# Performance work log

Hardware: AMD Instinct MI355X
Metric: run time of the kernel (lower is better)

Reference implementation:

```python
import jax, jax.numpy as jnp
import numpy as np

H = 100  # hidden size of both LSTM layers (fixed in the module)

def lstm_layer(x, w_ih, w_hh, b_ih, b_hh):
    # x: [B, T, I]; w_ih: [4H, I]; w_hh: [4H, H]; biases: [4H]
    # PyTorch gate order: input, forget, cell(g), output.
    B, T, _ = x.shape
    xg = jnp.einsum('bti,gi->btg', x, w_ih) + b_ih + b_hh  # [B, T, 4H], input GEMM hoisted out of the scan
    h0 = jnp.zeros((B, H), x.dtype)
    c0 = jnp.zeros((B, H), x.dtype)
    w_hh_t = w_hh.T  # [H, 4H]

    def step(carry, xg_t):
        h, c = carry
        g = xg_t + h @ w_hh_t                # [B, 4H]
        i, f, gg, o = jnp.split(g, 4, axis=-1)
        i = jax.nn.sigmoid(i)
        f = jax.nn.sigmoid(f)
        gg = jnp.tanh(gg)
        o = jax.nn.sigmoid(o)
        c = f * c + i * gg
        h = o * jnp.tanh(c)
        return (h, c), h

    _, hs = jax.lax.scan(step, (h0, c0), jnp.swapaxes(xg, 0, 1))  # hs: [T, B, H]
    return jnp.swapaxes(hs, 0, 1)  # [B, T, H]


def setup_inputs() -> dict:
    key = jax.random.key(0)
    ks = jax.random.split(key, 13)
    B, T, I = 256, 2048, 8
    s = lambda fan: 1.0 / np.sqrt(fan)
    u = lambda k, shape, fan: jax.random.uniform(k, shape, jnp.float32, -s(fan), s(fan))
    return {
        'x': jax.random.normal(ks[0], (B, T, I), jnp.float32),
        'w_ih1': u(ks[1], (4 * H, I), H), 'w_hh1': u(ks[2], (4 * H, H), H),
        'b_ih1': u(ks[3], (4 * H,), H), 'b_hh1': u(ks[4], (4 * H,), H),
        'w_ih2': u(ks[5], (4 * H, H), H), 'w_hh2': u(ks[6], (4 * H, H), H),
        'b_ih2': u(ks[7], (4 * H,), H), 'b_hh2': u(ks[8], (4 * H,), H),
        'fc1_w': u(ks[9], (25, H), H), 'fc1_b': u(ks[10], (25,), H),
        'fc2_w': u(ks[11], (1, 25), 25), 'fc2_b': u(ks[12], (1,), 25),
    }


def reference(x, w_ih1, w_hh1, b_ih1, b_hh1, w_ih2, w_hh2, b_ih2, b_hh2,
              fc1_w, fc1_b, fc2_w, fc2_b):
    # Dropout layers are identity in eval mode.
    h1 = lstm_layer(x, w_ih1, w_hh1, b_ih1, b_hh1)    # [B, T, H]
    h2 = lstm_layer(h1, w_ih2, w_hh2, b_ih2, b_hh2)   # [B, T, H]
    last = h2[:, -1, :]                               # [B, H]
    y = last @ fc1_w.T + fc1_b                        # [B, 25]
    return y @ fc2_w.T + fc2_b                        # [B, 1]
```

## Files before the change

### kernel.cpp

```cpp
#include <hip/hip_runtime.h>

#define BB 256
#define TT 2048
#define HD 100
#define NGP 448

typedef _Float16 h2v __attribute__((ext_vector_type(2)));

__device__ __forceinline__ float fdot2s(unsigned w, unsigned h, float c) {
#if __has_builtin(__builtin_amdgcn_fdot2)
    return __builtin_amdgcn_fdot2(__builtin_bit_cast(h2v, w),
                                  __builtin_bit_cast(h2v, h), c, false);
#else
    h2v av = __builtin_bit_cast(h2v, w), bv = __builtin_bit_cast(h2v, h);
    c = fmaf((float)av[0], (float)bv[0], c);
    c = fmaf((float)av[1], (float)bv[1], c);
    return c;
#endif
}
__device__ __forceinline__ unsigned packh2(float a, float b) {
    h2v p; p[0] = (_Float16)a; p[1] = (_Float16)b;
    return __builtin_bit_cast(unsigned, p);
}
__device__ __forceinline__ float sigmoid_f(float x) {
    return 1.0f / (1.0f + __expf(-x));
}
__device__ __forceinline__ float tanh_f(float x) {
    return 1.0f - 2.0f / (__expf(2.0f * x) + 1.0f);
}

__global__ __launch_bounds__(960, 1) void lstm_fused(
    const float* __restrict__ x,
    const float* __restrict__ w_ih1, const float* __restrict__ w_hh1,
    const float* __restrict__ b_ih1, const float* __restrict__ b_hh1,
    const float* __restrict__ w_ih2, const float* __restrict__ w_hh2,
    const float* __restrict__ b_ih2, const float* __restrict__ b_hh2,
    const float* __restrict__ fc1_w, const float* __restrict__ fc1_b,
    const float* __restrict__ fc2_w, const float* __restrict__ fc2_b,
    float* __restrict__ out)
{
    const int b    = blockIdx.x;
    const int tid  = threadIdx.x;
    const int lane = tid & 63;

    __shared__ unsigned h1p[64];
    __shared__ unsigned h2p[64];
    __shared__ __align__(16) unsigned xb[2][32][4];
    __shared__ float g1[NGP];
    __shared__ float g2[NGP];
    __shared__ float h2f[HD];
    __shared__ float fca[25];

    const bool isL1 = (tid < NGP);
    const bool isL2 = (tid >= NGP && tid < 2 * NGP);
    const bool isLd = (tid >= 896 && tid < 928);
    const bool isU1 = (tid < 50);
    const int  u2m  = tid - NGP;
    const bool isU2 = (u2m >= 0 && u2m < 50);

    const int g    = isL2 ? (tid - NGP) : tid;
    const int blk  = g / 112;
    const int r    = g - blk * 112;
    const int srow = blk * HD + r;
    const bool real = (isL1 || isL2) && (r < HD);

    unsigned wx[4];
    unsigned wa[50], wb[50];
    float bias = 0.0f;
    float c0 = 0.0f, c1 = 0.0f;

    wx[0] = wx[1] = wx[2] = wx[3] = 0u;
    #pragma unroll
    for (int q = 0; q < 50; ++q) { wa[q] = 0u; wb[q] = 0u; }

    if (isL1 && real) {
        const float4* ip = (const float4*)(w_ih1 + (size_t)srow * 8);
        float4 v0 = ip[0], v1 = ip[1];
        wx[0] = packh2(v0.x, v0.y); wx[1] = packh2(v0.z, v0.w);
        wx[2] = packh2(v1.x, v1.y); wx[3] = packh2(v1.z, v1.w);
        const float4* hp = (const float4*)(w_hh1 + (size_t)srow * HD);
        #pragma unroll
        for (int q = 0; q < 25; ++q) {
            float4 v = hp[q];
            wa[2*q]   = packh2(v.x, v.y);
            wa[2*q+1] = packh2(v.z, v.w);
        }
        bias = b_ih1[srow] + b_hh1[srow];
    }
    if (isL2 && real) {
        const float4* ip = (const float4*)(w_ih2 + (size_t)srow * HD);
        #pragma unroll
        for (int q = 0; q < 25; ++q) {
            float4 v = ip[q];
            wa[2*q]   = packh2(v.x, v.y);
            wa[2*q+1] = packh2(v.z, v.w);
        }
        const float4* hp = (const float4*)(w_hh2 + (size_t)srow * HD);
        #pragma unroll
        for (int q = 0; q < 25; ++q) {
            float4 v = hp[q];
            wb[2*q]   = packh2(v.x, v.y);
            wb[2*q+1] = packh2(v.z, v.w);
        }
        bias = b_ih2[srow] + b_hh2[srow];
    }

    if (tid < 64) { h1p[tid] = 0u; h2p[tid] = 0u; }
    if (isLd) {
        const int s = tid - 896;
        const float4* xp = (const float4*)(x + ((size_t)b * TT + s) * 8);
        float4 a0v = xp[0], a1v = xp[1];
        xb[0][s][0] = packh2(a0v.x, a0v.y); xb[0][s][1] = packh2(a0v.z, a0v.w);
        xb[0][s][2] = packh2(a1v.x, a1v.y); xb[0][s][3] = packh2(a1v.z, a1v.w);
    }
    __syncthreads();

    float4 pa = {0,0,0,0}, pb = {0,0,0,0};

    #pragma unroll 1
    for (int i = 0; i <= TT; ++i) {
        const bool pf = ((i & 31) == 0) && (i + 32 < TT);
        if (isL1 && i < TT) {
            unsigned st = h1p[lane];
            const uint4 xq = *((const uint4*)xb[(i >> 5) & 1][i & 31]);
            float a0 = bias, a1 = 0.0f;
            a0 = fdot2s(wx[0], xq.x, a0);
            a1 = fdot2s(wx[1], xq.y, a1);
            a0 = fdot2s(wx[2], xq.z, a0);
            a1 = fdot2s(wx[3], xq.w, a1);
            #pragma unroll
            for (int k = 0; k < 50; ++k) {
                unsigned hk = (unsigned)__builtin_amdgcn_readlane((int)st, k);
                if (k & 1) a1 = fdot2s(wa[k], hk, a1);
                else       a0 = fdot2s(wa[k], hk, a0);
            }
            float acc = a0 + a1;
            g1[g] = (blk == 2) ? tanh_f(acc) : sigmoid_f(acc);
        }
        if (isLd && pf) {
            const float4* xp = (const float4*)(x + ((size_t)b * TT + (i + 32) + (tid - 896)) * 8);
            pa = xp[0]; pb = xp[1];
        }
        if (isL2 && i >= 1) {
            unsigned st1 = h1p[lane];
            unsigned st2 = h2p[lane];
            float a0 = bias, a1 = 0.0f;
            #pragma unroll
            for (int k = 0; k < 50; ++k) {
                unsigned hk = (unsigned)__builtin_amdgcn_readlane((int)st1, k);
                if (k & 1) a1 = fdot2s(wa[k], hk, a1);
                else       a0 = fdot2s(wa[k], hk, a0);
            }
            #pragma unroll
            for (int k = 0; k < 50; ++k) {
                unsigned hk = (unsigned)__builtin_amdgcn_readlane((int)st2, k);
                if (k & 1) a1 = fdot2s(wb[k], hk, a1);
                else       a0 = fdot2s(wb[k], hk, a0);
            }
            float acc = a0 + a1;
            g2[g] = (blk == 2) ? tanh_f(acc) : sigmoid_f(acc);
        }
        __syncthreads();
        if (isU1 && i < TT) {
            const int m = tid;
            float2 iv = *(const float2*)(g1 + 2*m);
            float2 fv = *(const float2*)(g1 + 112 + 2*m);
            float2 gv = *(const float2*)(g1 + 224 + 2*m);
            float2 ov = *(const float2*)(g1 + 336 + 2*m);
            c0 = fv.x * c0 + iv.x * gv.x;
            c1 = fv.y * c1 + iv.y * gv.y;
            float h0 = ov.x * tanh_f(c0);
            float h1 = ov.y * tanh_f(c1);
            h1p[m] = packh2(h0, h1);
        }
        if (isU2 && i >= 1) {
            const int m = u2m;
            float2 iv = *(const float2*)(g2 + 2*m);
            float2 fv = *(const float2*)(g2 + 112 + 2*m);
            float2 gv = *(const float2*)(g2 + 224 + 2*m);
            float2 ov = *(const float2*)(g2 + 336 + 2*m);
            c0 = fv.x * c0 + iv.x * gv.x;
            c1 = fv.y * c1 + iv.y * gv.y;
            float h0 = ov.x * tanh_f(c0);
            float h1 = ov.y * tanh_f(c1);
            h2p[m] = packh2(h0, h1);
            if (i == TT) { h2f[2*m] = h0; h2f[2*m+1] = h1; }
        }
        if (isLd && pf) {
            const int s  = tid - 896;
            const int nb = ((i >> 5) + 1) & 1;
            xb[nb][s][0] = packh2(pa.x, pa.y); xb[nb][s][1] = packh2(pa.z, pa.w);
            xb[nb][s][2] = packh2(pb.x, pb.y); xb[nb][s][3] = packh2(pb.z, pb.w);
        }
        __syncthreads();
    }

    if (tid < 25) {
        float a = fc1_b[tid];
        const float* wp = fc1_w + tid * HD;
        #pragma unroll
        for (int k = 0; k < HD; ++k) a += h2f[k] * wp[k];
        fca[tid] = a;
    }
    __syncthreads();
    if (tid == 0) {
        float y = fc2_b[0];
        #pragma unroll
        for (int m = 0; m < 25; ++m) y += fca[m] * fc2_w[m];
        out[b] = y;
    }
}

extern "C" void kernel_launch(void* const* d_in, const int* in_sizes, int n_in,
                              void* d_out, int out_size, void* d_ws, size_t ws_size,
                              hipStream_t stream) {
    const float* x     = (const float*)d_in[0];
    const float* w_ih1 = (const float*)d_in[1];
    const float* w_hh1 = (const float*)d_in[2];
    const float* b_ih1 = (const float*)d_in[3];
    const float* b_hh1 = (const float*)d_in[4];
    const float* w_ih2 = (const float*)d_in[5];
    const float* w_hh2 = (const float*)d_in[6];
    const float* b_ih2 = (const float*)d_in[7];
    const float* b_hh2 = (const float*)d_in[8];
    const float* fc1_w = (const float*)d_in[9];
    const float* fc1_b = (const float*)d_in[10];
    const float* fc2_w = (const float*)d_in[11];
    const float* fc2_b = (const float*)d_in[12];
    float* out = (float*)d_out;

    lstm_fused<<<BB, 960, 0, stream>>>(x, w_ih1, w_hh1, b_ih1, b_hh1,
                                       w_ih2, w_hh2, b_ih2, b_hh2,
                                       fc1_w, fc1_b, fc2_w, fc2_b, out);
}
```

Measured before the change: 3.393 ms.

## Split fused two-layer LSTM into chunked per-layer kernels with two gates per thread

Replaces the single 960-thread fused kernel with alternating layer-1 and layer-2 kernels over time chunks. Each kernel uses 256 threads, and each thread computes two gate rows, so fewer waves share a barrier. Layer-1 hidden states for a chunk go through a global workspace and are prefetched by layer 2. Cell and hidden state carry across chunks through memory. The FC head moves to its own kernel. The layers no longer overlap in time, and the change adds launch overhead and global round trips in exchange for smaller blocks and cheaper barriers.

After: 4.307 ms. +26.9%, slower.

```diff
diff --git a/kernel.cpp b/kernel.cpp
--- a/kernel.cpp
+++ b/kernel.cpp
@@ -3,18 +3,17 @@
 #define BB 256
 #define TT 2048
 #define HD 100
-#define NGP 448
 
 typedef _Float16 h2v __attribute__((ext_vector_type(2)));
 
-__device__ __forceinline__ float fdot2s(unsigned w, unsigned h, float c) {
+__device__ __forceinline__ float fdot2(unsigned w, unsigned h, float c) {
 #if __has_builtin(__builtin_amdgcn_fdot2)
     return __builtin_amdgcn_fdot2(__builtin_bit_cast(h2v, w),
                                   __builtin_bit_cast(h2v, h), c, false);
 #else
-    h2v av = __builtin_bit_cast(h2v, w), bv = __builtin_bit_cast(h2v, h);
-    c = fmaf((float)av[0], (float)bv[0], c);
-    c = fmaf((float)av[1], (float)bv[1], c);
+    h2v a = __builtin_bit_cast(h2v, w), b = __builtin_bit_cast(h2v, h);
+    c = fmaf((float)a[0], (float)b[0], c);
+    c = fmaf((float)a[1], (float)b[1], c);
     return c;
 #endif
 }
@@ -22,193 +21,259 @@
     h2v p; p[0] = (_Float16)a; p[1] = (_Float16)b;
     return __builtin_bit_cast(unsigned, p);
 }
-__device__ __forceinline__ float sigmoid_f(float x) {
-    return 1.0f / (1.0f + __expf(-x));
-}
-__device__ __forceinline__ float tanh_f(float x) {
-    return 1.0f - 2.0f / (__expf(2.0f * x) + 1.0f);
-}
-
-__global__ __launch_bounds__(960, 1) void lstm_fused(
+__device__ __forceinline__ float sigmoid_f(float x) { return 1.0f / (1.0f + __expf(-x)); }
+__device__ __forceinline__ float tanh_f(float x)    { return 1.0f - 2.0f / (__expf(2.0f * x) + 1.0f); }
+
+__global__ __launch_bounds__(256, 1) void lstm_l1(
     const float* __restrict__ x,
-    const float* __restrict__ w_ih1, const float* __restrict__ w_hh1,
-    const float* __restrict__ b_ih1, const float* __restrict__ b_hh1,
-    const float* __restrict__ w_ih2, const float* __restrict__ w_hh2,
-    const float* __restrict__ b_ih2, const float* __restrict__ b_hh2,
-    const float* __restrict__ fc1_w, const float* __restrict__ fc1_b,
-    const float* __restrict__ fc2_w, const float* __restrict__ fc2_b,
-    float* __restrict__ out)
+    const float* __restrict__ w_ih, const float* __restrict__ w_hh,
+    const float* __restrict__ b_ih, const float* __restrict__ b_hh,
+    unsigned* __restrict__ h1buf,
+    float* __restrict__ c1s,
+    int t0, int Tc, int first)
 {
-    const int b    = blockIdx.x;
-    const int tid  = threadIdx.x;
-    const int lane = tid & 63;
-
+    const int b = blockIdx.x, tid = threadIdx.x, lane = tid & 63;
     __shared__ unsigned h1p[64];
+    __shared__ float glds[400];
+    __shared__ unsigned xs[2][32][4];
+
+    const bool isG = tid < 200;
+    const int  gt  = isG ? tid : 199;
+    const int  um  = tid >> 2;
+    const bool isU = ((tid & 3) == 3) && (tid < 200);
+    const bool isX = ((tid & 3) == 1) && (tid < 128);
+
+    unsigned wA[54], wB[54];
+    float bias0, bias1, cc0 = 0.f, cc1 = 0.f;
+
+    {
+        const int g0 = 2 * gt, g1 = 2 * gt + 1;
+        { const float4* p = (const float4*)(w_ih + (size_t)g0 * 8);
+          float4 v0 = p[0], v1 = p[1];
+          wA[0] = packh2(v0.x, v0.y); wA[1] = packh2(v0.z, v0.w);
+          wA[2] = packh2(v1.x, v1.y); wA[3] = packh2(v1.z, v1.w); }
+        { const float4* p = (const float4*)(w_ih + (size_t)g1 * 8);
+          float4 v0 = p[0], v1 = p[1];
+          wB[0] = packh2(v0.x, v0.y); wB[1] = packh2(v0.z, v0.w);
+          wB[2] = packh2(v1.x, v1.y); wB[3] = packh2(v1.z, v1.w); }
+        { const float4* p = (const float4*)(w_hh + (size_t)g0 * HD);
+          #pragma unroll
+          for (int q = 0; q < 25; ++q) {
+              float4 v = p[q];
+              wA[4 + 2*q] = packh2(v.x, v.y); wA[5 + 2*q] = packh2(v.z, v.w);
+          } }
+        { const float4* p = (const float4*)(w_hh + (size_t)g1 * HD);
+          #pragma unroll
+          for (int q = 0; q < 25; ++q) {
+              float4 v = p[q];
+              wB[4 + 2*q] = packh2(v.x, v.y); wB[5 + 2*q] = packh2(v.z, v.w);
+          } }
+        bias0 = b_ih[g0] + b_hh[g0];
+        bias1 = b_ih[g1] + b_hh[g1];
+    }
+    if (isU && !first) {
+        cc0 = c1s[b * HD + 2 * um];
+        cc1 = c1s[b * HD + 2 * um + 1];
+    }
+    if (tid < 64) {
+        unsigned v = 0u;
+        if (!first && tid < 50) v = h1buf[((size_t)(Tc - 1) * BB + b) * 50 + tid];
+        h1p[tid] = v;
+    }
+    if (isX) {
+        const int s = um;
+        const float4* p = (const float4*)(x + ((size_t)b * TT + t0 + s) * 8);
+        float4 v0 = p[0], v1 = p[1];
+        xs[0][s][0] = packh2(v0.x, v0.y); xs[0][s][1] = packh2(v0.z, v0.w);
+        xs[0][s][2] = packh2(v1.x, v1.y); xs[0][s][3] = packh2(v1.z, v1.w);
+    }
+    __syncthreads();
+
+    float4 pa = {0,0,0,0}, pb = {0,0,0,0};
+
+    #pragma unroll 1
+    for (int i = 0; i < Tc; ++i) {
+        const bool pf = ((i & 31) == 0) && (i + 32 < Tc) && isX;
+        if (pf) {
+            const float4* p = (const float4*)(x + ((size_t)b * TT + t0 + i + 32 + um) * 8);
+            pa = p[0]; pb = p[1];
+        }
+        const unsigned st = h1p[lane];
+        const unsigned* xq = xs[(i >> 5) & 1][i & 31];
+        unsigned x0 = xq[0], x1 = xq[1], x2 = xq[2], x3 = xq[3];
+        float a0 = bias0, a1 = bias1, a2 = 0.f, a3 = 0.f;
+        a0 = fdot2(wA[0], x0, a0); a1 = fdot2(wB[0], x0, a1);
+        a2 = fdot2(wA[1], x1, a2); a3 = fdot2(wB[1], x1, a3);
+        a0 = fdot2(wA[2], x2, a0); a1 = fdot2(wB[2], x2, a1);
+        a2 = fdot2(wA[3], x3, a2); a3 = fdot2(wB[3], x3, a3);
+        #pragma unroll
+        for (int k = 0; k < 50; ++k) {
+            unsigned hk = (unsigned)__builtin_amdgcn_readlane((int)st, k);
+            if (k & 1) { a2 = fdot2(wA[4 + k], hk, a2); a3 = fdot2(wB[4 + k], hk, a3); }
+            else       { a0 = fdot2(wA[4 + k], hk, a0); a1 = fdot2(wB[4 + k], hk, a1); }
+        }
+        float r0 = a0 + a2, r1 = a1 + a3;
+        const bool tg = (tid >= 100) && (tid < 150);
+        r0 = tg ? tanh_f(r0) : sigmoid_f(r0);
+        r1 = tg ? tanh_f(r1) : sigmoid_f(r1);
+        if (isG) *(float2*)(glds + 2 * tid) = make_float2(r0, r1);
+        __syncthreads();
+        if (isU) {
+            const int j = 2 * um;
+            float2 gi = *(const float2*)(glds + j);
+            float2 gf = *(const float2*)(glds + 100 + j);
+            float2 gg = *(const float2*)(glds + 200 + j);
+            float2 go = *(const float2*)(glds + 300 + j);
+            cc0 = gf.x * cc0 + gi.x * gg.x;
+            cc1 = gf.y * cc1 + gi.y * gg.y;
+            float h0 = go.x * tanh_f(cc0);
+            float h1v = go.y * tanh_f(cc1);
+            unsigned hp = packh2(h0, h1v);
+            h1p[um] = hp;
+            h1buf[((size_t)i * BB + b) * 50 + um] = hp;
+            if (i == Tc - 1) { c1s[b * HD + j] = cc0; c1s[b * HD + j + 1] = cc1; }
+        }
+        if (pf) {
+            const int nb2 = ((i >> 5) + 1) & 1; const int s = um;
+            xs[nb2][s][0] = packh2(pa.x, pa.y); xs[nb2][s][1] = packh2(pa.z, pa.w);
+            xs[nb2][s][2] = packh2(pb.x, pb.y); xs[nb2][s][3] = packh2(pb.z, pb.w);
+        }
+        __syncthreads();
+    }
+}
+
+__global__ __launch_bounds__(256, 1) void lstm_l2(
+    const unsigned* __restrict__ h1buf,
+    const float* __restrict__ w_ih, const float* __restrict__ w_hh,
+    const float* __restrict__ b_ih, const float* __restrict__ b_hh,
+    unsigned* __restrict__ h2sp,
+    float* __restrict__ c2s,
+    float* __restrict__ h2f,
+    int Tc, int first, int last)
+{
+    const int b = blockIdx.x, tid = threadIdx.x, lane = tid & 63;
     __shared__ unsigned h2p[64];
-    __shared__ __align__(16) unsigned xb[2][32][4];
-    __shared__ float g1[NGP];
-    __shared__ float g2[NGP];
-    __shared__ float h2f[HD];
-    __shared__ float fca[25];
-
-    const bool isL1 = (tid < NGP);
-    const bool isL2 = (tid >= NGP && tid < 2 * NGP);
-    const bool isLd = (tid >= 896 && tid < 928);
-    const bool isU1 = (tid < 50);
-    const int  u2m  = tid - NGP;
-    const bool isU2 = (u2m >= 0 && u2m < 50);
-
-    const int g    = isL2 ? (tid - NGP) : tid;
-    const int blk  = g / 112;
-    const int r    = g - blk * 112;
-    const int srow = blk * HD + r;
-    const bool real = (isL1 || isL2) && (r < HD);
-
-    unsigned wx[4];
-    unsigned wa[50], wb[50];
-    float bias = 0.0f;
-    float c0 = 0.0f, c1 = 0.0f;
-
-    wx[0] = wx[1] = wx[2] = wx[3] = 0u;
+    __shared__ float glds[400];
+
+    const bool isG = tid < 200;
+    const int  gt  = isG ? tid : 199;
+    const int  um  = tid >> 2;
+    const bool isU = ((tid & 3) == 3) && (tid < 200);
+
+    unsigned wIA[50], wIB[50], wHA[50], wHB[50];
+    float bias0, bias1, cc0 = 0.f, cc1 = 0.f;
+
+    {
+        const int g0 = 2 * gt, g1 = 2 * gt + 1;
+        { const float4* p = (const float4*)(w_ih + (size_t)g0 * HD);
+          #pragma unroll
+          for (int q = 0; q < 25; ++q) {
+              float4 v = p[q];
+              wIA[2*q] = packh2(v.x, v.y); wIA[2*q+1] = packh2(v.z, v.w);
+          } }
+        { const float4* p = (const float4*)(w_ih + (size_t)g1 * HD);
+          #pragma unroll
+          for (int q = 0; q < 25; ++q) {
+              float4 v = p[q];
+              wIB[2*q] = packh2(v.x, v.y); wIB[2*q+1] = packh2(v.z, v.w);
+          } }
+        { const float4* p = (const float4*)(w_hh + (size_t)g0 * HD);
+          #pragma unroll
+          for (int q = 0; q < 25; ++q) {
+              float4 v = p[q];
+              wHA[2*q] = packh2(v.x, v.y); wHA[2*q+1] = packh2(v.z, v.w);
+          } }
+        { const float4* p = (const float4*)(w_hh + (size_t)g1 * HD);
+          #pragma unroll
+          for (int q = 0; q < 25; ++q) {
+              float4 v = p[q];
+              wHB[2*q] = packh2(v.x, v.y); wHB[2*q+1] = packh2(v.z, v.w);
+          } }
+        bias0 = b_ih[g0] + b_hh[g0];
+        bias1 = b_ih[g1] + b_hh[g1];
+    }
+    if (isU && !first) {
+        cc0 = c2s[b * HD + 2 * um];
+        cc1 = c2s[b * HD + 2 * um + 1];
+    }
+    if (tid < 64) {
+        unsigned v = 0u;
+        if (!first && tid < 50) v = h2sp[b * 50 + tid];
+        h2p[tid] = v;
+    }
+    const int lidx = (lane < 50) ? lane : 49;
+    unsigned cur = h1buf[(size_t)b * 50 + lidx];
+    __syncthreads();
+
+    #pragma unroll 1
+    for (int i = 0; i < Tc; ++i) {
+        const int tn = (i + 1 < Tc) ? (i + 1) : i;
+        unsigned nxt = h1buf[((size_t)tn * BB + b) * 50 + lidx];
+        const unsigned st2 = h2p[lane];
+        float a0 = bias0, a1 = bias1, a2 = 0.f, a3 = 0.f;
+        #pragma unroll
+        for (int k = 0; k < 50; ++k) {
+            unsigned hk = (unsigned)__builtin_amdgcn_readlane((int)cur, k);
+            if (k & 1) { a2 = fdot2(wIA[k], hk, a2); a3 = fdot2(wIB[k], hk, a3); }
+            else       { a0 = fdot2(wIA[k], hk, a0); a1 = fdot2(wIB[k], hk, a1); }
+        }
+        #pragma unroll
+        for (int k = 0; k < 50; ++k) {
+            unsigned hk = (unsigned)__builtin_amdgcn_readlane((int)st2, k);
+            if (k & 1) { a2 = fdot2(wHA[k], hk, a2); a3 = fdot2(wHB[k], hk, a3); }
+            else       { a0 = fdot2(wHA[k], hk, a0); a1 = fdot2(wHB[k], hk, a1); }
+        }
+        float r0 = a0 + a2, r1 = a1 + a3;
+        const bool tg = (tid >= 100) && (tid < 150);
+        r0 = tg ? tanh_f(r0) : sigmoid_f(r0);
+        r1 = tg ? tanh_f(r1) : sigmoid_f(r1);
+        if (isG) *(float2*)(glds + 2 * tid) = make_float2(r0, r1);
+        __syncthreads();
+        if (isU) {
+            const int j = 2 * um;
+            float2 gi = *(const float2*)(glds + j);
+            float2 gf = *(const float2*)(glds + 100 + j);
+            float2 gg = *(const float2*)(glds + 200 + j);
+            float2 go = *(const float2*)(glds + 300 + j);
+            cc0 = gf.x * cc0 + gi.x * gg.x;
+            cc1 = gf.y * cc1 + gi.y * gg.y;
+            float h0 = go.x * tanh_f(cc0);
+            float h1v = go.y * tanh_f(cc1);
+            h2p[um] = packh2(h0, h1v);
+            if (i == Tc - 1) {
+                h2sp[b * 50 + um] = packh2(h0, h1v);
+                c2s[b * HD + j] = cc0; c2s[b * HD + j + 1] = cc1;
+                if (last) { h2f[b * HD + j] = h0; h2f[b * HD + j + 1] = h1v; }
+            }
+        }
+        __syncthreads();
+        cur = nxt;
+    }
+}
+
+__global__ void fc_head(const float* __restrict__ h2,
+                        const float* __restrict__ fc1_w, const float* __restrict__ fc1_b,
+                        const float* __restrict__ fc2_w, const float* __restrict__ fc2_b,
+                        float* __restrict__ out)
+{
+    const int bidx = threadIdx.x;
+    const float* h = h2 + (size_t)bidx * HD;
+    float hv[HD];
     #pragma unroll
-    for (int q = 0; q < 50; ++q) { wa[q] = 0u; wb[q] = 0u; }
-
-    if (isL1 && real) {
-        const float4* ip = (const float4*)(w_ih1 + (size_t)srow * 8);
-        float4 v0 = ip[0], v1 = ip[1];
-        wx[0] = packh2(v0.x, v0.y); wx[1] = packh2(v0.z, v0.w);
-        wx[2] = packh2(v1.x, v1.y); wx[3] = packh2(v1.z, v1.w);
-        const float4* hp = (const float4*)(w_hh1 + (size_t)srow * HD);
+    for (int kk = 0; kk < HD/4; ++kk) {
+        float4 v = *(const float4*)(h + 4*kk);
+        hv[4*kk+0]=v.x; hv[4*kk+1]=v.y; hv[4*kk+2]=v.z; hv[4*kk+3]=v.w;
+    }
+    float y = fc2_b[0];
+    #pragma unroll
+    for (int m = 0; m < 25; ++m) {
+        float a = fc1_b[m];
+        const float* wp = fc1_w + m * HD;
         #pragma unroll
-        for (int q = 0; q < 25; ++q) {
-            float4 v = hp[q];
-            wa[2*q]   = packh2(v.x, v.y);
-            wa[2*q+1] = packh2(v.z, v.w);
-        }
-        bias = b_ih1[srow] + b_hh1[srow];
-    }
-    if (isL2 && real) {
-        const float4* ip = (const float4*)(w_ih2 + (size_t)srow * HD);
-        #pragma unroll
-        for (int q = 0; q < 25; ++q) {
-            float4 v = ip[q];
-            wa[2*q]   = packh2(v.x, v.y);
-            wa[2*q+1] = packh2(v.z, v.w);
-        }
-        const float4* hp = (const float4*)(w_hh2 + (size_t)srow * HD);
-        #pragma unroll
-        for (int q = 0; q < 25; ++q) {
-            float4 v = hp[q];
-            wb[2*q]   = packh2(v.x, v.y);
-            wb[2*q+1] = packh2(v.z, v.w);
-        }
-        bias = b_ih2[srow] + b_hh2[srow];
-    }
-
-    if (tid < 64) { h1p[tid] = 0u; h2p[tid] = 0u; }
-    if (isLd) {
-        const int s = tid - 896;
-        const float4* xp = (const float4*)(x + ((size_t)b * TT + s) * 8);
-        float4 a0v = xp[0], a1v = xp[1];
-        xb[0][s][0] = packh2(a0v.x, a0v.y); xb[0][s][1] = packh2(a0v.z, a0v.w);
-        xb[0][s][2] = packh2(a1v.x, a1v.y); xb[0][s][3] = packh2(a1v.z, a1v.w);
-    }
-    __syncthreads();
-
-    float4 pa = {0,0,0,0}, pb = {0,0,0,0};
-
-    #pragma unroll 1
-    for (int i = 0; i <= TT; ++i) {
-        const bool pf = ((i & 31) == 0) && (i + 32 < TT);
-        if (isL1 && i < TT) {
-            unsigned st = h1p[lane];
-            const uint4 xq = *((const uint4*)xb[(i >> 5) & 1][i & 31]);
-            float a0 = bias, a1 = 0.0f;
-            a0 = fdot2s(wx[0], xq.x, a0);
-            a1 = fdot2s(wx[1], xq.y, a1);
-            a0 = fdot2s(wx[2], xq.z, a0);
-            a1 = fdot2s(wx[3], xq.w, a1);
-            #pragma unroll
-            for (int k = 0; k < 50; ++k) {
-                unsigned hk = (unsigned)__builtin_amdgcn_readlane((int)st, k);
-                if (k & 1) a1 = fdot2s(wa[k], hk, a1);
-                else       a0 = fdot2s(wa[k], hk, a0);
-            }
-            float acc = a0 + a1;
-            g1[g] = (blk == 2) ? tanh_f(acc) : sigmoid_f(acc);
-        }
-        if (isLd && pf) {
-            const float4* xp = (const float4*)(x + ((size_t)b * TT + (i + 32) + (tid - 896)) * 8);
-            pa = xp[0]; pb = xp[1];
-        }
-        if (isL2 && i >= 1) {
-            unsigned st1 = h1p[lane];
-            unsigned st2 = h2p[lane];
-            float a0 = bias, a1 = 0.0f;
-            #pragma unroll
-            for (int k = 0; k < 50; ++k) {
-                unsigned hk = (unsigned)__builtin_amdgcn_readlane((int)st1, k);
-                if (k & 1) a1 = fdot2s(wa[k], hk, a1);
-                else       a0 = fdot2s(wa[k], hk, a0);
-            }
-            #pragma unroll
-            for (int k = 0; k < 50; ++k) {
-                unsigned hk = (unsigned)__builtin_amdgcn_readlane((int)st2, k);
-                if (k & 1) a1 = fdot2s(wb[k], hk, a1);
-                else       a0 = fdot2s(wb[k], hk, a0);
-            }
-            float acc = a0 + a1;
-            g2[g] = (blk == 2) ? tanh_f(acc) : sigmoid_f(acc);
-        }
-        __syncthreads();
-        if (isU1 && i < TT) {
-            const int m = tid;
-            float2 iv = *(const float2*)(g1 + 2*m);
-            float2 fv = *(const float2*)(g1 + 112 + 2*m);
-            float2 gv = *(const float2*)(g1 + 224 + 2*m);
-            float2 ov = *(const float2*)(g1 + 336 + 2*m);
-            c0 = fv.x * c0 + iv.x * gv.x;
-            c1 = fv.y * c1 + iv.y * gv.y;
-            float h0 = ov.x * tanh_f(c0);
-            float h1 = ov.y * tanh_f(c1);
-            h1p[m] = packh2(h0, h1);
-        }
-        if (isU2 && i >= 1) {
-            const int m = u2m;
-            float2 iv = *(const float2*)(g2 + 2*m);
-            float2 fv = *(const float2*)(g2 + 112 + 2*m);
-            float2 gv = *(const float2*)(g2 + 224 + 2*m);
-            float2 ov = *(const float2*)(g2 + 336 + 2*m);
-            c0 = fv.x * c0 + iv.x * gv.x;
-            c1 = fv.y * c1 + iv.y * gv.y;
-            float h0 = ov.x * tanh_f(c0);
-            float h1 = ov.y * tanh_f(c1);
-            h2p[m] = packh2(h0, h1);
-            if (i == TT) { h2f[2*m] = h0; h2f[2*m+1] = h1; }
-        }
-        if (isLd && pf) {
-            const int s  = tid - 896;
-            const int nb = ((i >> 5) + 1) & 1;
-            xb[nb][s][0] = packh2(pa.x, pa.y); xb[nb][s][1] = packh2(pa.z, pa.w);
-            xb[nb][s][2] = packh2(pb.x, pb.y); xb[nb][s][3] = packh2(pb.z, pb.w);
-        }
-        __syncthreads();
-    }
-
-    if (tid < 25) {
-        float a = fc1_b[tid];
-        const float* wp = fc1_w + tid * HD;
-        #pragma unroll
-        for (int k = 0; k < HD; ++k) a += h2f[k] * wp[k];
-        fca[tid] = a;
-    }
-    __syncthreads();
-    if (tid == 0) {
-        float y = fc2_b[0];
-        #pragma unroll
-        for (int m = 0; m < 25; ++m) y += fca[m] * fc2_w[m];
-        out[b] = y;
-    }
+        for (int k = 0; k < HD; ++k) a += hv[k] * wp[k];
+        y += a * fc2_w[m];
+    }
+    out[bidx] = y;
 }
 
 extern "C" void kernel_launch(void* const* d_in, const int* in_sizes, int n_in,
@@ -229,7 +294,21 @@
     const float* fc2_b = (const float*)d_in[12];
     float* out = (float*)d_out;
 
-    lstm_fused<<<BB, 960, 0, stream>>>(x, w_ih1, w_hh1, b_ih1, b_hh1,
-                                       w_ih2, w_hh2, b_ih2, b_hh2,
-                                       fc1_w, fc1_b, fc2_w, fc2_b, out);
-}
+    int Tc = 256;
+    while (Tc > 32 && (size_t)Tc * BB * 50 * 4 + (size_t)BB * (HD * 3 + 50) * 4 > ws_size) Tc >>= 1;
+
+    unsigned* h1buf = (unsigned*)d_ws;
+    float* c1s = (float*)(h1buf + (size_t)Tc * BB * 50);
+    float* c2s = c1s + (size_t)BB * HD;
+    float* h2f = c2s + (size_t)BB * HD;
+    unsigned* h2sp = (unsigned*)(h2f + (size_t)BB * HD);
+
+    const int nch = TT / Tc;
+    for (int ch = 0; ch < nch; ++ch) {
+        lstm_l1<<<BB, 256, 0, stream>>>(x, w_ih1, w_hh1, b_ih1, b_hh1,
+                                        h1buf, c1s, ch * Tc, Tc, ch == 0);
+        lstm_l2<<<BB, 256, 0, stream>>>(h1buf, w_ih2, w_hh2, b_ih2, b_hh2,
+                                        h2sp, c2s, h2f, Tc, ch == 0, ch == nch - 1);
+    }
+    fc_head<<<1, 256, 0, stream>>>(h2f, fc1_w, fc1_b, fc2_w, fc2_b, out);
+}
```

## Compute two gate rows per thread with 512-thread blocks and unified activation

Applied to the files above, without the earlier changes.

Remaps work so each thread computes two adjacent gate rows, with all weights held in 200 packed-half registers, and shrinks the block from 960 to 512 threads split into two 256-thread layer groups. The per-gate sigmoid/tanh branch is replaced by one branch-free activation built from fmaf and a hardware reciprocal. Gate buffers are compacted to 400 entries, and the cell update is spread across lanes with stride 4. This aims to cut wave count and per-step barrier cost, at the price of heavy register pressure (possible spills) and less parallelism per step.

Result: faster. 2.771 ms (-18.3%).

```diff
diff --git a/kernel.cpp b/kernel.cpp
--- a/kernel.cpp
+++ b/kernel.cpp
@@ -3,18 +3,17 @@
 #define BB 256
 #define TT 2048
 #define HD 100
-#define NGP 448
 
 typedef _Float16 h2v __attribute__((ext_vector_type(2)));
 
-__device__ __forceinline__ float fdot2s(unsigned w, unsigned h, float c) {
+__device__ __forceinline__ float fdot2(unsigned w, unsigned h, float c) {
 #if __has_builtin(__builtin_amdgcn_fdot2)
     return __builtin_amdgcn_fdot2(__builtin_bit_cast(h2v, w),
                                   __builtin_bit_cast(h2v, h), c, false);
 #else
-    h2v av = __builtin_bit_cast(h2v, w), bv = __builtin_bit_cast(h2v, h);
-    c = fmaf((float)av[0], (float)bv[0], c);
-    c = fmaf((float)av[1], (float)bv[1], c);
+    h2v a = __builtin_bit_cast(h2v, w), b = __builtin_bit_cast(h2v, h);
+    c = fmaf((float)a[0], (float)b[0], c);
+    c = fmaf((float)a[1], (float)b[1], c);
     return c;
 #endif
 }
@@ -22,14 +21,21 @@
     h2v p; p[0] = (_Float16)a; p[1] = (_Float16)b;
     return __builtin_bit_cast(unsigned, p);
 }
-__device__ __forceinline__ float sigmoid_f(float x) {
-    return 1.0f / (1.0f + __expf(-x));
+__device__ __forceinline__ float rcp_f(float x) {
+#if __has_builtin(__builtin_amdgcn_rcpf)
+    return __builtin_amdgcn_rcpf(x);
+#else
+    return 1.0f / x;
+#endif
+}
+__device__ __forceinline__ float act_f(float x, float m, float s, float d) {
+    return fmaf(m, rcp_f(1.0f + __expf(-s * x)), d);
 }
 __device__ __forceinline__ float tanh_f(float x) {
-    return 1.0f - 2.0f / (__expf(2.0f * x) + 1.0f);
-}
-
-__global__ __launch_bounds__(960, 1) void lstm_fused(
+    return fmaf(2.0f, rcp_f(1.0f + __expf(-2.0f * x)), -1.0f);
+}
+
+__global__ __launch_bounds__(512, 1) void lstm_fused(
     const float* __restrict__ x,
     const float* __restrict__ w_ih1, const float* __restrict__ w_hh1,
     const float* __restrict__ b_ih1, const float* __restrict__ b_hh1,
@@ -42,76 +48,90 @@
     const int b    = blockIdx.x;
     const int tid  = threadIdx.x;
     const int lane = tid & 63;
+    const int grp  = tid >> 8;
+    const int lt   = tid & 255;
 
     __shared__ unsigned h1p[64];
     __shared__ unsigned h2p[64];
-    __shared__ __align__(16) unsigned xb[2][32][4];
-    __shared__ float g1[NGP];
-    __shared__ float g2[NGP];
+    __shared__ __align__(16) unsigned xs[2][32][4];
+    __shared__ float g1[400];
+    __shared__ float g2[400];
     __shared__ float h2f[HD];
     __shared__ float fca[25];
 
-    const bool isL1 = (tid < NGP);
-    const bool isL2 = (tid >= NGP && tid < 2 * NGP);
-    const bool isLd = (tid >= 896 && tid < 928);
-    const bool isU1 = (tid < 50);
-    const int  u2m  = tid - NGP;
-    const bool isU2 = (u2m >= 0 && u2m < 50);
-
-    const int g    = isL2 ? (tid - NGP) : tid;
-    const int blk  = g / 112;
-    const int r    = g - blk * 112;
-    const int srow = blk * HD + r;
-    const bool real = (isL1 || isL2) && (r < HD);
-
-    unsigned wx[4];
-    unsigned wa[50], wb[50];
-    float bias = 0.0f;
-    float c0 = 0.0f, c1 = 0.0f;
-
-    wx[0] = wx[1] = wx[2] = wx[3] = 0u;
-    #pragma unroll
-    for (int q = 0; q < 50; ++q) { wa[q] = 0u; wb[q] = 0u; }
-
-    if (isL1 && real) {
-        const float4* ip = (const float4*)(w_ih1 + (size_t)srow * 8);
-        float4 v0 = ip[0], v1 = ip[1];
-        wx[0] = packh2(v0.x, v0.y); wx[1] = packh2(v0.z, v0.w);
-        wx[2] = packh2(v1.x, v1.y); wx[3] = packh2(v1.z, v1.w);
-        const float4* hp = (const float4*)(w_hh1 + (size_t)srow * HD);
-        #pragma unroll
-        for (int q = 0; q < 25; ++q) {
-            float4 v = hp[q];
-            wa[2*q]   = packh2(v.x, v.y);
-            wa[2*q+1] = packh2(v.z, v.w);
-        }
-        bias = b_ih1[srow] + b_hh1[srow];
-    }
-    if (isL2 && real) {
-        const float4* ip = (const float4*)(w_ih2 + (size_t)srow * HD);
-        #pragma unroll
-        for (int q = 0; q < 25; ++q) {
-            float4 v = ip[q];
-            wa[2*q]   = packh2(v.x, v.y);
-            wa[2*q+1] = packh2(v.z, v.w);
-        }
-        const float4* hp = (const float4*)(w_hh2 + (size_t)srow * HD);
-        #pragma unroll
-        for (int q = 0; q < 25; ++q) {
-            float4 v = hp[q];
-            wb[2*q]   = packh2(v.x, v.y);
-            wb[2*q+1] = packh2(v.z, v.w);
-        }
-        bias = b_ih2[srow] + b_hh2[srow];
-    }
+    const bool isG = lt < 200;
+    const int  gt  = isG ? lt : 199;
+    const int  um  = lt >> 2;
+    const bool isU = ((lt & 3) == 3) && isG;
+    const bool isX = (grp == 0) && (lt >= 200) && (lt < 232);
+    const int  xsl = lt - 200;
+
+    unsigned wreg[200];
+    float bias0, bias1, cc0 = 0.f, cc1 = 0.f;
+
+    const int g0 = 2 * gt, g1r = 2 * gt + 1;
+    if (grp == 0) {
+        { const float4* p = (const float4*)(w_ih1 + (size_t)g0 * 8);
+          float4 v0 = p[0], v1 = p[1];
+          wreg[0] = packh2(v0.x, v0.y); wreg[1] = packh2(v0.z, v0.w);
+          wreg[2] = packh2(v1.x, v1.y); wreg[3] = packh2(v1.z, v1.w); }
+        { const float4* p = (const float4*)(w_ih1 + (size_t)g1r * 8);
+          float4 v0 = p[0], v1 = p[1];
+          wreg[54] = packh2(v0.x, v0.y); wreg[55] = packh2(v0.z, v0.w);
+          wreg[56] = packh2(v1.x, v1.y); wreg[57] = packh2(v1.z, v1.w); }
+        { const float4* p = (const float4*)(w_hh1 + (size_t)g0 * HD);
+          #pragma unroll
+          for (int q = 0; q < 25; ++q) {
+              float4 v = p[q];
+              wreg[4 + 2*q] = packh2(v.x, v.y); wreg[5 + 2*q] = packh2(v.z, v.w);
+          } }
+        { const float4* p = (const float4*)(w_hh1 + (size_t)g1r * HD);
+          #pragma unroll
+          for (int q = 0; q < 25; ++q) {
+              float4 v = p[q];
+              wreg[58 + 2*q] = packh2(v.x, v.y); wreg[59 + 2*q] = packh2(v.z, v.w);
+          } }
+        bias0 = b_ih1[g0] + b_hh1[g0];
+        bias1 = b_ih1[g1r] + b_hh1[g1r];
+    } else {
+        { const float4* p = (const float4*)(w_ih2 + (size_t)g0 * HD);
+          #pragma unroll
+          for (int q = 0; q < 25; ++q) {
+              float4 v = p[q];
+              wreg[2*q] = packh2(v.x, v.y); wreg[2*q + 1] = packh2(v.z, v.w);
+          } }
+        { const float4* p = (const float4*)(w_ih2 + (size_t)g1r * HD);
+          #pragma unroll
+          for (int q = 0; q < 25; ++q) {
+              float4 v = p[q];
+              wreg[50 + 2*q] = packh2(v.x, v.y); wreg[51 + 2*q] = packh2(v.z, v.w);
+          } }
+        { const float4* p = (const float4*)(w_hh2 + (size_t)g0 * HD);
+          #pragma unroll
+          for (int q = 0; q < 25; ++q) {
+              float4 v = p[q];
+              wreg[100 + 2*q] = packh2(v.x, v.y); wreg[101 + 2*q] = packh2(v.z, v.w);
+          } }
+        { const float4* p = (const float4*)(w_hh2 + (size_t)g1r * HD);
+          #pragma unroll
+          for (int q = 0; q < 25; ++q) {
+              float4 v = p[q];
+              wreg[150 + 2*q] = packh2(v.x, v.y); wreg[151 + 2*q] = packh2(v.z, v.w);
+          } }
+        bias0 = b_ih2[g0] + b_hh2[g0];
+        bias1 = b_ih2[g1r] + b_hh2[g1r];
+    }
+    const bool tg = (gt >= 100) && (gt < 150);
+    const float am = tg ? 2.0f : 1.0f;
+    const float as = tg ? 2.0f : 1.0f;
+    const float ad = tg ? -1.0f : 0.0f;
 
     if (tid < 64) { h1p[tid] = 0u; h2p[tid] = 0u; }
-    if (isLd) {
-        const int s = tid - 896;
-        const float4* xp = (const float4*)(x + ((size_t)b * TT + s) * 8);
-        float4 a0v = xp[0], a1v = xp[1];
-        xb[0][s][0] = packh2(a0v.x, a0v.y); xb[0][s][1] = packh2(a0v.z, a0v.w);
-        xb[0][s][2] = packh2(a1v.x, a1v.y); xb[0][s][3] = packh2(a1v.z, a1v.w);
+    if (isX) {
+        const float4* p = (const float4*)(x + ((size_t)b * TT + xsl) * 8);
+        float4 v0 = p[0], v1 = p[1];
+        xs[0][xsl][0] = packh2(v0.x, v0.y); xs[0][xsl][1] = packh2(v0.z, v0.w);
+        xs[0][xsl][2] = packh2(v1.x, v1.y); xs[0][xsl][3] = packh2(v1.z, v1.w);
     }
     __syncthreads();
 
@@ -120,77 +140,87 @@
     #pragma unroll 1
     for (int i = 0; i <= TT; ++i) {
         const bool pf = ((i & 31) == 0) && (i + 32 < TT);
-        if (isL1 && i < TT) {
-            unsigned st = h1p[lane];
-            const uint4 xq = *((const uint4*)xb[(i >> 5) & 1][i & 31]);
-            float a0 = bias, a1 = 0.0f;
-            a0 = fdot2s(wx[0], xq.x, a0);
-            a1 = fdot2s(wx[1], xq.y, a1);
-            a0 = fdot2s(wx[2], xq.z, a0);
-            a1 = fdot2s(wx[3], xq.w, a1);
-            #pragma unroll
-            for (int k = 0; k < 50; ++k) {
-                unsigned hk = (unsigned)__builtin_amdgcn_readlane((int)st, k);
-                if (k & 1) a1 = fdot2s(wa[k], hk, a1);
-                else       a0 = fdot2s(wa[k], hk, a0);
-            }
-            float acc = a0 + a1;
-            g1[g] = (blk == 2) ? tanh_f(acc) : sigmoid_f(acc);
-        }
-        if (isLd && pf) {
-            const float4* xp = (const float4*)(x + ((size_t)b * TT + (i + 32) + (tid - 896)) * 8);
-            pa = xp[0]; pb = xp[1];
-        }
-        if (isL2 && i >= 1) {
-            unsigned st1 = h1p[lane];
-            unsigned st2 = h2p[lane];
-            float a0 = bias, a1 = 0.0f;
-            #pragma unroll
-            for (int k = 0; k < 50; ++k) {
-                unsigned hk = (unsigned)__builtin_amdgcn_readlane((int)st1, k);
-                if (k & 1) a1 = fdot2s(wa[k], hk, a1);
-                else       a0 = fdot2s(wa[k], hk, a0);
-            }
-            #pragma unroll
-            for (int k = 0; k < 50; ++k) {
-                unsigned hk = (unsigned)__builtin_amdgcn_readlane((int)st2, k);
-                if (k & 1) a1 = fdot2s(wb[k], hk, a1);
-                else       a0 = fdot2s(wb[k], hk, a0);
-            }
-            float acc = a0 + a1;
-            g2[g] = (blk == 2) ? tanh_f(acc) : sigmoid_f(acc);
+        if (grp == 0) {
+            if (i < TT) {
+                if (isX && pf) {
+                    const float4* p = (const float4*)(x + ((size_t)b * TT + i + 32 + xsl) * 8);
+                    pa = p[0]; pb = p[1];
+                }
+                const unsigned st = h1p[lane];
+                const unsigned* xq = xs[(i >> 5) & 1][i & 31];
+                unsigned x0 = xq[0], x1 = xq[1], x2 = xq[2], x3 = xq[3];
+                float a0 = bias0, a1 = bias1, a2 = 0.f, a3 = 0.f;
+                a0 = fdot2(wreg[0], x0, a0); a2 = fdot2(wreg[1], x1, a2);
+                a0 = fdot2(wreg[2], x2, a0); a2 = fdot2(wreg[3], x3, a2);
+                a1 = fdot2(wreg[54], x0, a1); a3 = fdot2(wreg[55], x1, a3);
+                a1 = fdot2(wreg[56], x2, a1); a3 = fdot2(wreg[57], x3, a3);
+                #pragma unroll
+                for (int k = 0; k < 50; ++k) {
+                    unsigned hk = (unsigned)__builtin_amdgcn_readlane((int)st, k);
+                    if (k & 1) { a2 = fdot2(wreg[4 + k], hk, a2); a3 = fdot2(wreg[58 + k], hk, a3); }
+                    else       { a0 = fdot2(wreg[4 + k], hk, a0); a1 = fdot2(wreg[58 + k], hk, a1); }
+                }
+                float r0 = act_f(a0 + a2, am, as, ad);
+                float r1 = act_f(a1 + a3, am, as, ad);
+                if (isG) *(float2*)(g1 + 2 * gt) = make_float2(r0, r1);
+            }
+        } else {
+            if (i >= 1) {
+                const unsigned cur = h1p[lane];
+                const unsigned st2 = h2p[lane];
+                float a0 = bias0, a1 = bias1, a2 = 0.f, a3 = 0.f;
+                #pragma unroll
+                for (int k = 0; k < 50; ++k) {
+                    unsigned hk = (unsigned)__builtin_amdgcn_readlane((int)cur, k);
+                    if (k & 1) { a2 = fdot2(wreg[k], hk, a2); a3 = fdot2(wreg[50 + k], hk, a3); }
+                    else       { a0 = fdot2(wreg[k], hk, a0); a1 = fdot2(wreg[50 + k], hk, a1); }
+                }
+                #pragma unroll
+                for (int k = 0; k < 50; ++k) {
+                    unsigned hk = (unsigned)__builtin_amdgcn_readlane((int)st2, k);
+                    if (k & 1) { a2 = fdot2(wreg[100 + k], hk, a2); a3 = fdot2(wreg[150 + k], hk, a3); }
+                    else       { a0 = fdot2(wreg[100 + k], hk, a0); a1 = fdot2(wreg[150 + k], hk, a1); }
+                }
+                float r0 = act_f(a0 + a2, am, as, ad);
+                float r1 = act_f(a1 + a3, am, as, ad);
+                if (isG) *(float2*)(g2 + 2 * gt) = make_float2(r0, r1);
+            }
         }
         __syncthreads();
-        if (isU1 && i < TT) {
-            const int m = tid;
-            float2 iv = *(const float2*)(g1 + 2*m);
-            float2 fv = *(const float2*)(g1 + 112 + 2*m);
-            float2 gv = *(const float2*)(g1 + 224 + 2*m);
-            float2 ov = *(const float2*)(g1 + 336 + 2*m);
-            c0 = fv.x * c0 + iv.x * gv.x;
-            c1 = fv.y * c1 + iv.y * gv.y;
-            float h0 = ov.x * tanh_f(c0);
-            float h1 = ov.y * tanh_f(c1);
-            h1p[m] = packh2(h0, h1);
-        }
-        if (isU2 && i >= 1) {
-            const int m = u2m;
-            float2 iv = *(const float2*)(g2 + 2*m);
-            float2 fv = *(const float2*)(g2 + 112 + 2*m);
-            float2 gv = *(const float2*)(g2 + 224 + 2*m);
-            float2 ov = *(const float2*)(g2 + 336 + 2*m);
-            c0 = fv.x * c0 + iv.x * gv.x;
-            c1 = fv.y * c1 + iv.y * gv.y;
-            float h0 = ov.x * tanh_f(c0);
-            float h1 = ov.y * tanh_f(c1);
-            h2p[m] = packh2(h0, h1);
-            if (i == TT) { h2f[2*m] = h0; h2f[2*m+1] = h1; }
-        }
-        if (isLd && pf) {
-            const int s  = tid - 896;
-            const int nb = ((i >> 5) + 1) & 1;
-            xb[nb][s][0] = packh2(pa.x, pa.y); xb[nb][s][1] = packh2(pa.z, pa.w);
-            xb[nb][s][2] = packh2(pb.x, pb.y); xb[nb][s][3] = packh2(pb.z, pb.w);
+        if (grp == 0) {
+            if (i < TT) {
+                if (isU) {
+                    const int j = 2 * um;
+                    float2 gi = *(const float2*)(g1 + j);
+                    float2 gf = *(const float2*)(g1 + 100 + j);
+                    float2 gg = *(const float2*)(g1 + 200 + j);
+                    float2 go = *(const float2*)(g1 + 300 + j);
+                    cc0 = gf.x * cc0 + gi.x * gg.x;
+                    cc1 = gf.y * cc1 + gi.y * gg.y;
+                    float h0 = go.x * tanh_f(cc0);
+                    float h1v = go.y * tanh_f(cc1);
+                    h1p[um] = packh2(h0, h1v);
+                }
+                if (isX && pf) {
+                    const int nb2 = ((i >> 5) + 1) & 1;
+                    xs[nb2][xsl][0] = packh2(pa.x, pa.y); xs[nb2][xsl][1] = packh2(pa.z, pa.w);
+                    xs[nb2][xsl][2] = packh2(pb.x, pb.y); xs[nb2][xsl][3] = packh2(pb.z, pb.w);
+                }
+            }
+        } else {
+            if (i >= 1 && isU) {
+                const int j = 2 * um;
+                float2 gi = *(const float2*)(g2 + j);
+                float2 gf = *(const float2*)(g2 + 100 + j);
+                float2 gg = *(const float2*)(g2 + 200 + j);
+                float2 go = *(const float2*)(g2 + 300 + j);
+                cc0 = gf.x * cc0 + gi.x * gg.x;
+                cc1 = gf.y * cc1 + gi.y * gg.y;
+                float h0 = go.x * tanh_f(cc0);
+                float h1v = go.y * tanh_f(cc1);
+                h2p[um] = packh2(h0, h1v);
+                if (i == TT) { h2f[j] = h0; h2f[j + 1] = h1v; }
+            }
         }
         __syncthreads();
     }
@@ -229,7 +259,7 @@
     const float* fc2_b = (const float*)d_in[12];
     float* out = (float*)d_out;
 
-    lstm_fused<<<BB, 960, 0, stream>>>(x, w_ih1, w_hh1, b_ih1, b_hh1,
+    lstm_fused<<<BB, 512, 0, stream>>>(x, w_ih1, w_hh1, b_ih1, b_hh1,
                                        w_ih2, w_hh2, b_ih2, b_hh2,
                                        fc1_w, fc1_b, fc2_w, fc2_b, out);
 }
```
